# Kernel optimization log

Measured on AMD Instinct MI355X. Metric: run time of the kernel, lower is better.

Reference implementation:

```python
import jax, jax.numpy as jnp
import numpy as np

D = 256        # model_dim
E = 4          # num_experts
H = 8          # attention heads
L = 8          # layers
P = 4          # patch size
IMG = 128
B = 8
NUM_CLASSES = 10
T = (IMG // P) ** 2  # 1024 tokens


def _ln(x, g, b):
    mu = jnp.mean(x, -1, keepdims=True)
    var = jnp.mean((x - mu) ** 2, -1, keepdims=True)
    return (x - mu) * jax.lax.rsqrt(var + 1e-5) * g + b


def setup_inputs() -> dict:
    key = jax.random.key(0)
    ks = jax.random.split(key, 24)
    n = lambda k, s, sc=0.02: jax.random.normal(k, s, jnp.float32) * sc
    return {
        "x": jax.random.normal(ks[0], (B, 3, IMG, IMG), jnp.float32),
        "patch_w": n(ks[1], (D, 3, P, P), 0.1),
        "patch_b": n(ks[2], (D,), 0.01),
        "pos_emb": n(ks[3], (1, T, D), 0.02),
        "router_w": n(ks[4], (E, D), 0.05),
        "router_b": n(ks[5], (E,), 0.01),
        "ln1_g": jnp.ones((L, D), jnp.float32),
        "ln1_b": jnp.zeros((L, D), jnp.float32),
        "q_w": n(ks[6], (L, D, D), 0.05),
        "q_b": n(ks[7], (L, D), 0.01),
        "k_w": n(ks[8], (L, D, D), 0.05),
        "k_b": n(ks[9], (L, D), 0.01),
        "v_w": n(ks[10], (L, D, D), 0.05),
        "v_b": n(ks[11], (L, D), 0.01),
        "o_w": n(ks[12], (L, D, D), 0.05),
        "o_b": n(ks[13], (L, D), 0.01),
        "ln2_g": jnp.ones((L, D), jnp.float32),
        "ln2_b": jnp.zeros((L, D), jnp.float32),
        "l1_w": n(ks[14], (L, 4 * D, D), 0.05),
        "l1_b": n(ks[15], (L, 4 * D), 0.01),
        "l2_w": n(ks[16], (L, D, 4 * D), 0.05),
        "l2_b": n(ks[17], (L, D), 0.01),
        "head_w": n(ks[18], (NUM_CLASSES, D), 0.05),
        "head_b": n(ks[19], (NUM_CLASSES,), 0.01),
        "alpha": jnp.full((1,), 0.5, jnp.float32),
    }


def reference(x, patch_w, patch_b, pos_emb, router_w, router_b, ln1_g, ln1_b,
              q_w, q_b, k_w, k_b, v_w, v_b, o_w, o_b, ln2_g, ln2_b,
              l1_w, l1_b, l2_w, l2_b, head_w, head_b, alpha):
    b = x.shape[0]
    # patch embed: Conv2d(3, D, P, stride=P)
    h = jax.lax.conv_general_dilated(x, patch_w, (P, P), 'VALID',
                                     dimension_numbers=('NCHW', 'OIHW', 'NCHW'))
    h = h + patch_b[None, :, None, None]
    tok = h.reshape(b, D, -1).transpose(0, 2, 1) + pos_emb   # [B,T,D]
    t = tok.shape[1]
    n_per = t // E  # uniform capacity: floor(T * 1/E)
    raw_prob = jax.nn.softmax(tok @ router_w.T + router_b, axis=-1)  # [B,T,E]
    # greedy routing: expert e takes top n_per of remaining tokens, rows zeroed after
    prob = raw_prob
    bidx = jnp.arange(b)[:, None]
    blocks, pblocks = [], []
    for e in range(E):
        _, idx = jax.lax.top_k(prob[:, :, e], n_per)            # [B,n_per]
        blocks.append(jnp.take_along_axis(tok, idx[:, :, None], axis=1))
        pblocks.append(jnp.take_along_axis(raw_prob, idx[:, :, None], axis=1))
        sel = jnp.zeros((b, t), prob.dtype).at[bidx, idx].set(1.0)
        prob = prob * (1.0 - sel)[:, :, None]
    xs = jnp.concatenate(blocks, axis=1)    # [B,T,D] expert-sorted
    rp = jnp.concatenate(pblocks, axis=1)   # [B,T,E]

    widths = [D // 2 ** e for e in range(E)]  # [256,128,64,32]
    scale = D ** -0.5                         # note: model_dim, not head_dim
    dh = D // H
    for l in range(L):
        # ---- nested-expert MHSA ----
        xn = _ln(xs, ln1_g[l], ln1_b[l])
        qs, ks_, vs = [], [], []
        for e in range(E):
            m = widths[e]
            blk = xn[:, e * n_per:(e + 1) * n_per, :m]
            qs.append(blk @ q_w[l][:, :m].T + q_b[l])
            ks_.append(blk @ k_w[l][:, :m].T + k_b[l])
            vs.append(blk @ v_w[l][:, :m].T + v_b[l])
        q = jnp.concatenate(qs, 1).reshape(b, t, H, dh).transpose(0, 2, 1, 3)
        k = jnp.concatenate(ks_, 1).reshape(b, t, H, dh).transpose(0, 2, 1, 3)
        v = jnp.concatenate(vs, 1).reshape(b, t, H, dh).transpose(0, 2, 1, 3)
        attn = jax.nn.softmax(jnp.einsum('bhqd,bhkd->bhqk', q, k) * scale, axis=-1)
        ao = jnp.einsum('bhqk,bhkd->bhqd', attn, v).transpose(0, 2, 1, 3).reshape(b, t, D)
        outs = []
        for e in range(E):
            m = widths[e]
            sl = slice(e * n_per, (e + 1) * n_per)
            o = ao[:, sl, :m] @ o_w[l][:m, :m].T + o_b[l][:m]
            o = jnp.pad(o, ((0, 0), (0, 0), (0, D - m)))
            outs.append(o + xs[:, sl, :])
        xs = jnp.concatenate(outs, 1)
        # ---- nested-expert MLP ----
        xn = _ln(xs, ln2_g[l], ln2_b[l])
        outs = []
        for e in range(E):
            m = widths[e]
            sl = slice(e * n_per, (e + 1) * n_per)
            blk = xn[:, sl, :m]
            inner = jax.nn.gelu(blk @ l1_w[l][:, :m].T + l1_b[l], approximate=False)
            outer = inner @ l2_w[l][:m, :].T + l2_b[l][:m]
            outer = jnp.pad(outer, ((0, 0), (0, 0), (0, D - m)))
            sf = (alpha[0] * rp[:, sl, e] + 1.0)[:, :, None]
            outs.append(xs[:, sl, :] + sf * outer)
        xs = jnp.concatenate(outs, 1)
    # classification head: mean pool + linear
    return jnp.mean(xs, axis=1) @ head_w.T + head_b
```

## Files before the change

### kernel.cpp

```cpp
#include <hip/hip_runtime.h>
#include <math.h>

#define D 256
#define E 4
#define H 8
#define LYR 8
#define IMG 128
#define BB 8
#define NC 10
#define T 1024
#define NPER 256
#define DH 32
#define D4 1024

using bf16x8 = __attribute__((ext_vector_type(8))) __bf16;
using bf16x4 = __attribute__((ext_vector_type(4))) __bf16;
using f32x4  = __attribute__((ext_vector_type(4))) float;

#define MFMA16(a, b, c) __builtin_amdgcn_mfma_f32_16x16x32_bf16((a), (b), (c), 0, 0, 0)

__global__ void cast6(const float* __restrict__ s0, const float* __restrict__ s1,
                      const float* __restrict__ s2, const float* __restrict__ s3,
                      const float* __restrict__ s4, const float* __restrict__ s5,
                      __bf16* __restrict__ d0, __bf16* __restrict__ d1,
                      __bf16* __restrict__ d2, __bf16* __restrict__ d3,
                      __bf16* __restrict__ d4, __bf16* __restrict__ d5) {
    const long A4 = (long)LYR * D * D / 4;
    const long W4 = (long)LYR * D4 * D / 4;
    long i = (long)blockIdx.x * 256 + threadIdx.x;
    const float* s; __bf16* d; long off;
    if (i < 4 * A4) {
        int w = (int)(i / A4); off = i - (long)w * A4;
        s = w == 0 ? s0 : w == 1 ? s1 : w == 2 ? s2 : s3;
        d = w == 0 ? d0 : w == 1 ? d1 : w == 2 ? d2 : d3;
    } else {
        long j = i - 4 * A4;
        int w = (int)(j / W4); off = j - (long)w * W4;
        s = w ? s5 : s4; d = w ? d5 : d4;
    }
    float4 v = ((const float4*)s)[off];
    bf16x4 o;
    o[0] = (__bf16)v.x; o[1] = (__bf16)v.y; o[2] = (__bf16)v.z; o[3] = (__bf16)v.w;
    ((bf16x4*)d)[off] = o;
}

__global__ void patch_embed(const float* __restrict__ x, const float* __restrict__ pw,
                            const float* __restrict__ pb, const float* __restrict__ pos,
                            float* __restrict__ tok) {
    int t = blockIdx.x, b = blockIdx.y, d = threadIdx.x;
    __shared__ float sx[48];
    int ph = t >> 5, pwc = t & 31;
    if (d < 48) {
        int c = d >> 4, ij = d & 15, i = ij >> 2, j = ij & 3;
        sx[d] = x[(((long)b * 3 + c) * IMG + (ph * 4 + i)) * IMG + (pwc * 4 + j)];
    }
    __syncthreads();
    float acc = pb[d];
    #pragma unroll
    for (int kk = 0; kk < 48; ++kk) acc += sx[kk] * pw[d * 48 + kk];
    tok[((long)b * T + t) * D + d] = acc + pos[(long)t * D + d];
}

__global__ void router(const float* __restrict__ tok, const float* __restrict__ rw,
                       const float* __restrict__ rb, float* __restrict__ rawp) {
    int row = blockIdx.x;
    int lane = threadIdx.x;
    const float* tr = tok + (long)row * D;
    float a0 = 0.f, a1 = 0.f, a2 = 0.f, a3 = 0.f;
    for (int c = lane; c < D; c += 64) {
        float xv = tr[c];
        a0 += xv * rw[0 * D + c];
        a1 += xv * rw[1 * D + c];
        a2 += xv * rw[2 * D + c];
        a3 += xv * rw[3 * D + c];
    }
    for (int off = 32; off; off >>= 1) {
        a0 += __shfl_down(a0, off);
        a1 += __shfl_down(a1, off);
        a2 += __shfl_down(a2, off);
        a3 += __shfl_down(a3, off);
    }
    if (lane == 0) {
        float l0 = a0 + rb[0], l1 = a1 + rb[1], l2 = a2 + rb[2], l3 = a3 + rb[3];
        float mx = fmaxf(fmaxf(l0, l1), fmaxf(l2, l3));
        float e0 = __expf(l0 - mx), e1 = __expf(l1 - mx), e2 = __expf(l2 - mx), e3 = __expf(l3 - mx);
        float inv = 1.0f / (e0 + e1 + e2 + e3);
        rawp[(long)row * 4 + 0] = e0 * inv;
        rawp[(long)row * 4 + 1] = e1 * inv;
        rawp[(long)row * 4 + 2] = e2 * inv;
        rawp[(long)row * 4 + 3] = e3 * inv;
    }
}

__global__ __launch_bounds__(1024) void route_topk(const float* __restrict__ rawp,
                                                   int* __restrict__ perm,
                                                   float* __restrict__ rpsel) {
    int b = blockIdx.x, tid = threadIdx.x;
    int lane = tid & 63, wv = tid >> 6;
    __shared__ unsigned hist[256];
    __shared__ unsigned long long ball[16];
    __shared__ int sb_bin, sb_rem;
    bool assigned = false;
    for (int e = 0; e < E; ++e) {
        float v = rawp[((long)b * T + tid) * E + e];
        unsigned key = assigned ? 0u : __float_as_uint(v);
        unsigned prefix = 0;
        int rem = NPER;
        #pragma unroll
        for (int pass = 3; pass >= 0; --pass) {
            int shift = pass * 8;
            if (tid < 256) hist[tid] = 0;
            __syncthreads();
            bool active = (pass == 3) || ((key >> (shift + 8)) == prefix);
            if (active) atomicAdd(&hist[(key >> shift) & 255], 1u);
            __syncthreads();
            if (tid < 64) {
                unsigned c[4], psum = 0;
                #pragma unroll
                for (int u = 0; u < 4; ++u) { c[u] = hist[tid * 4 + u]; psum += c[u]; }
                unsigned suf = psum;
                #pragma unroll
                for (int off = 1; off < 64; off <<= 1) {
                    unsigned o = __shfl_down(suf, off);
                    if (tid + off < 64) suf += o;
                }
                unsigned El = suf - psum;
                if (El < (unsigned)rem && (unsigned)rem <= suf) {
                    unsigned cab = El;
                    #pragma unroll
                    for (int u = 3; u >= 0; --u) {
                        if ((unsigned)rem > cab && (unsigned)rem <= cab + c[u]) {
                            sb_bin = tid * 4 + u;
                            sb_rem = (int)((unsigned)rem - cab);
                        }
                        cab += c[u];
                    }
                }
            }
            __syncthreads();
            prefix = (prefix << 8) | (unsigned)sb_bin;
            rem = sb_rem;
        }
        unsigned t = prefix;
        bool is_tie = (!assigned) && (key == t);
        unsigned long long mbt = __ballot(is_tie);
        if (lane == 0) ball[wv] = mbt;
        __syncthreads();
        int tierank = 0;
        for (int w2 = 0; w2 < wv; ++w2) tierank += __popcll(ball[w2]);
        tierank += __popcll(mbt & ((1ULL << lane) - 1));
        bool sel = (!assigned) && ((key > t) || (is_tie && tierank < rem));
        __syncthreads();
        unsigned long long mbs = __ballot(sel);
        if (lane == 0) ball[wv] = mbs;
        __syncthreads();
        int rank = 0;
        for (int w2 = 0; w2 < wv; ++w2) rank += __popcll(ball[w2]);
        rank += __popcll(mbs & ((1ULL << lane) - 1));
        if (sel) {
            perm[(long)b * T + e * NPER + rank] = tid;
            rpsel[(long)b * T + e * NPER + rank] = v;
            assigned = true;
        }
        __syncthreads();
    }
}

__global__ void gather_tokens(const float* __restrict__ tok, const int* __restrict__ perm,
                              float* __restrict__ xs) {
    int slot = blockIdx.x, b = blockIdx.y, d = threadIdx.x;
    int src = perm[(long)b * T + slot];
    xs[((long)b * T + slot) * D + d] = tok[((long)b * T + src) * D + d];
}

__device__ __forceinline__ void ln_rows32(const float* __restrict__ src,
                                          const float* __restrict__ g,
                                          const float* __restrict__ bta,
                                          __bf16 (*slds)[264], int tid) {
    int sub = tid & 15, rowh = tid >> 4;
    int col0 = sub * 16;
    float gv[16], bv[16];
    #pragma unroll
    for (int u = 0; u < 4; ++u) {
        float4 gg = *(const float4*)&g[col0 + 4 * u];
        float4 bb = *(const float4*)&bta[col0 + 4 * u];
        gv[4*u] = gg.x; gv[4*u+1] = gg.y; gv[4*u+2] = gg.z; gv[4*u+3] = gg.w;
        bv[4*u] = bb.x; bv[4*u+1] = bb.y; bv[4*u+2] = bb.z; bv[4*u+3] = bb.w;
    }
    #pragma unroll
    for (int half = 0; half < 2; ++half) {
        int r = rowh + half * 16;
        const float* rp = src + (long)r * D + col0;
        float v[16];
        #pragma unroll
        for (int u = 0; u < 4; ++u) {
            float4 vv = *(const float4*)&rp[4 * u];
            v[4*u] = vv.x; v[4*u+1] = vv.y; v[4*u+2] = vv.z; v[4*u+3] = vv.w;
        }
        float s = 0.f;
        #pragma unroll
        for (int u = 0; u < 16; ++u) s += v[u];
        #pragma unroll
        for (int mk = 1; mk < 16; mk <<= 1) s += __shfl_xor(s, mk);
        float mu = s * (1.0f / D);
        float s2 = 0.f;
        #pragma unroll
        for (int u = 0; u < 16; ++u) { v[u] -= mu; s2 += v[u] * v[u]; }
        #pragma unroll
        for (int mk = 1; mk < 16; mk <<= 1) s2 += __shfl_xor(s2, mk);
        float rstd = rsqrtf(s2 * (1.0f / D) + 1e-5f);
        bf16x8 o0, o1;
        #pragma unroll
        for (int u = 0; u < 8; ++u) o0[u] = (__bf16)(v[u] * rstd * gv[u] + bv[u]);
        #pragma unroll
        for (int u = 0; u < 8; ++u) o1[u] = (__bf16)(v[8+u] * rstd * gv[8+u] + bv[8+u]);
        *(bf16x8*)&slds[r][col0]     = o0;
        *(bf16x8*)&slds[r][col0 + 8] = o1;
    }
}

__device__ __forceinline__ void gemm_tile(
    const __bf16* __restrict__ A, int lda,
    const __bf16* __restrict__ W, int ldb,
    int K, int lane, f32x4 acc[2][4])
{
    int lr = lane & 15, lk = (lane >> 4) * 8;
    const __bf16* a0 = A + (long)lr * lda + lk;
    const __bf16* a1 = a0 + 16 * lda;
    const __bf16* b0 = W + (long)lr * ldb + lk;
    const __bf16* b1 = b0 + 16 * ldb;
    const __bf16* b2 = b0 + 32 * ldb;
    const __bf16* b3 = b0 + 48 * ldb;
    #pragma unroll 2
    for (int k = 0; k < K; k += 32) {
        bf16x8 av0 = *(const bf16x8*)(a0 + k);
        bf16x8 av1 = *(const bf16x8*)(a1 + k);
        bf16x8 bv0 = *(const bf16x8*)(b0 + k);
        bf16x8 bv1 = *(const bf16x8*)(b1 + k);
        bf16x8 bv2 = *(const bf16x8*)(b2 + k);
        bf16x8 bv3 = *(const bf16x8*)(b3 + k);
        acc[0][0] = MFMA16(av0, bv0, acc[0][0]);
        acc[0][1] = MFMA16(av0, bv1, acc[0][1]);
        acc[0][2] = MFMA16(av0, bv2, acc[0][2]);
        acc[0][3] = MFMA16(av0, bv3, acc[0][3]);
        acc[1][0] = MFMA16(av1, bv0, acc[1][0]);
        acc[1][1] = MFMA16(av1, bv1, acc[1][1]);
        acc[1][2] = MFMA16(av1, bv2, acc[1][2]);
        acc[1][3] = MFMA16(av1, bv3, acc[1][3]);
    }
}

__global__ __launch_bounds__(256) void qkv_ln_gemm(
    const float* __restrict__ xs,
    const __bf16* __restrict__ qwb, const __bf16* __restrict__ kwb, const __bf16* __restrict__ vwb,
    const float* __restrict__ qb, const float* __restrict__ kb, const float* __restrict__ vb,
    const float* __restrict__ g, const float* __restrict__ bta,
    __bf16* __restrict__ Qb, __bf16* __restrict__ Kb, __bf16* __restrict__ Vt)
{
    int tid = threadIdx.x, lane = tid & 63, wid = tid >> 6;
    int tile = blockIdx.x, which = blockIdx.y, b = blockIdx.z;
    int row0 = tile * 32;
    int m = D >> (row0 >> 8);
    __shared__ __bf16 slds[32][264];
    ln_rows32(xs + ((long)b * T + row0) * D, g, bta, slds, tid);
    __syncthreads();
    const __bf16* W = which == 0 ? qwb : which == 1 ? kwb : vwb;
    const float* bias = which == 0 ? qb : which == 1 ? kb : vb;
    int ncol0 = wid * 64;
    const f32x4 vz = {0.f, 0.f, 0.f, 0.f};
    f32x4 acc[2][4];
    #pragma unroll
    for (int i = 0; i < 2; ++i) { acc[i][0]=vz; acc[i][1]=vz; acc[i][2]=vz; acc[i][3]=vz; }
    gemm_tile(&slds[0][0], 264, W + (long)ncol0 * D, D, m, lane, acc);
    int lr = lane & 15, rg = (lane >> 4) * 4;
    #pragma unroll
    for (int i = 0; i < 2; ++i) {
        int row = row0 + i * 16 + rg;
        #pragma unroll
        for (int j = 0; j < 4; ++j) {
            int n = ncol0 + j * 16 + lr;
            float bvs = bias[n];
            if (which == 2) {
                bf16x4 pk;
                #pragma unroll
                for (int r = 0; r < 4; ++r) pk[r] = (__bf16)(acc[i][j][r] + bvs);
                *(bf16x4*)&Vt[((long)b * D + n) * T + row] = pk;
            } else if (which == 0) {
                #pragma unroll
                for (int r = 0; r < 4; ++r)
                    Qb[((long)b * T + row + r) * D + n] = (__bf16)((acc[i][j][r] + bvs) * 0.0625f);
            } else {
                #pragma unroll
                for (int r = 0; r < 4; ++r)
                    Kb[((long)b * T + row + r) * D + n] = (__bf16)(acc[i][j][r] + bvs);
            }
        }
    }
}

__global__ __launch_bounds__(256) void attn_mfma(
    const __bf16* __restrict__ Qb, const __bf16* __restrict__ Kb,
    const __bf16* __restrict__ Vt, __bf16* __restrict__ aob)
{
    int bid = blockIdx.x;
    int bh = (bid & 7) * 8 + ((bid >> 3) & 7);
    int qt = bid >> 6;
    int b = bh >> 3, h = bh & 7;
    int lane = threadIdx.x & 63, wave = threadIdx.x >> 6;
    int lr = lane & 15, g = lane >> 4;
    int q0 = qt * 128 + wave * 32;
    __shared__ __bf16 plds[4][32][72];
    const f32x4 vz = {0.f, 0.f, 0.f, 0.f};
    bf16x8 qf[2];
    qf[0] = *(const bf16x8*)&Qb[((long)b * T + q0 + lr) * D + h * DH + g * 8];
    qf[1] = *(const bf16x8*)&Qb[((long)b * T + q0 + 16 + lr) * D + h * DH + g * 8];
    f32x4 acc[2][2] = {{vz, vz}, {vz, vz}};
    float ls[2] = {0.f, 0.f};
    const __bf16* kbase = Kb + (long)b * T * D + h * DH + g * 8;
    const __bf16* vbase = Vt + ((long)b * D + h * DH) * T;
    for (int kc = 0; kc < T; kc += 64) {
        bf16x8 kf[4];
        #pragma unroll
        for (int j = 0; j < 4; ++j)
            kf[j] = *(const bf16x8*)(kbase + (long)(kc + 16 * j + lr) * D);
        bf16x8 vf[2][2];
        #pragma unroll
        for (int w = 0; w < 2; ++w)
            #pragma unroll
            for (int df = 0; df < 2; ++df)
                vf[w][df] = *(const bf16x8*)(vbase + (long)(df * 16 + lr) * T + kc + 32 * w + 8 * g);
        #pragma unroll
        for (int qi = 0; qi < 2; ++qi) {
            #pragma unroll
            for (int j = 0; j < 4; ++j) {
                f32x4 s = MFMA16(kf[j], qf[qi], vz);
                float p0 = __expf(s[0]), p1 = __expf(s[1]);
                float p2 = __expf(s[2]), p3 = __expf(s[3]);
                ls[qi] += (p0 + p1) + (p2 + p3);
                bf16x4 pk;
                pk[0] = (__bf16)p0; pk[1] = (__bf16)p1;
                pk[2] = (__bf16)p2; pk[3] = (__bf16)p3;
                *(bf16x4*)&plds[wave][qi * 16 + lr][16 * j + 4 * g] = pk;
            }
        }
        #pragma unroll
        for (int qi = 0; qi < 2; ++qi) {
            #pragma unroll
            for (int w = 0; w < 2; ++w) {
                bf16x8 pa = *(const bf16x8*)&plds[wave][qi * 16 + lr][32 * w + 8 * g];
                acc[qi][0] = MFMA16(pa, vf[w][0], acc[qi][0]);
                acc[qi][1] = MFMA16(pa, vf[w][1], acc[qi][1]);
            }
        }
    }
    #pragma unroll
    for (int qi = 0; qi < 2; ++qi) {
        ls[qi] += __shfl_xor(ls[qi], 16);
        ls[qi] += __shfl_xor(ls[qi], 32);
        float inv = 1.0f / ls[qi];
        #pragma unroll
        for (int r = 0; r < 4; ++r) {
            float invr = __shfl(inv, 4 * g + r);
            long obase = ((long)b * T + q0 + qi * 16 + 4 * g + r) * D + h * DH;
            aob[obase + lr]      = (__bf16)(acc[qi][0][r] * invr);
            aob[obase + 16 + lr] = (__bf16)(acc[qi][1][r] * invr);
        }
    }
}

#define GEMM_PROLOGUE \
    int lane = threadIdx.x & 63, wid = threadIdx.x >> 6; \
    int wm = wid >> 1, wn = wid & 1; \
    int b = blockIdx.z >> 2, e = blockIdx.z & 3; \
    int m = D >> e; \
    const f32x4 vz = {0.f, 0.f, 0.f, 0.f}; \
    f32x4 acc[2][4]; \
    _Pragma("unroll") \
    for (int i = 0; i < 2; ++i) { acc[i][0]=vz; acc[i][1]=vz; acc[i][2]=vz; acc[i][3]=vz; }

__global__ __launch_bounds__(256) void oproj_gemm(
    const __bf16* __restrict__ aob, const __bf16* __restrict__ owb,
    const float* __restrict__ ob, float* __restrict__ xs)
{
    GEMM_PROLOGUE
    if ((int)blockIdx.y * 128 >= m) return;
    int ncol0 = blockIdx.y * 128 + wn * 64;
    int row0 = e * NPER + blockIdx.x * 64 + wm * 32;
    gemm_tile(aob + ((long)b * T + row0) * D, D, owb + (long)ncol0 * D, D, m, lane, acc);
    int lr = lane & 15, rg = (lane >> 4) * 4;
    #pragma unroll
    for (int i = 0; i < 2; ++i) {
        int row = row0 + i * 16 + rg;
        #pragma unroll
        for (int j = 0; j < 4; ++j) {
            int n = ncol0 + j * 16 + lr;
            if (n < m) {
                float bv = ob[n];
                #pragma unroll
                for (int r = 0; r < 4; ++r)
                    xs[((long)b * T + row + r) * D + n] += acc[i][j][r] + bv;
            }
        }
    }
}

__global__ __launch_bounds__(256) void mlp1_ln_gemm(
    const float* __restrict__ xs, const __bf16* __restrict__ w1b,
    const float* __restrict__ b1, const float* __restrict__ g, const float* __restrict__ bta,
    __bf16* __restrict__ innerb)
{
    int tid = threadIdx.x, lane = tid & 63, wid = tid >> 6;
    int tile = blockIdx.x, fq = blockIdx.y, b = blockIdx.z;
    int row0 = tile * 32;
    int m = D >> (row0 >> 8);
    __shared__ __bf16 slds[32][264];
    ln_rows32(xs + ((long)b * T + row0) * D, g, bta, slds, tid);
    __syncthreads();
    int ncol0 = fq * 256 + wid * 64;
    const f32x4 vz = {0.f, 0.f, 0.f, 0.f};
    f32x4 acc[2][4];
    #pragma unroll
    for (int i = 0; i < 2; ++i) { acc[i][0]=vz; acc[i][1]=vz; acc[i][2]=vz; acc[i][3]=vz; }
    gemm_tile(&slds[0][0], 264, w1b + (long)ncol0 * D, D, m, lane, acc);
    int lr = lane & 15, rg = (lane >> 4) * 4;
    #pragma unroll
    for (int i = 0; i < 2; ++i) {
        int row = row0 + i * 16 + rg;
        #pragma unroll
        for (int j = 0; j < 4; ++j) {
            int f = ncol0 + j * 16 + lr;
            float bv = b1[f];
            #pragma unroll
            for (int r = 0; r < 4; ++r) {
                float xv = acc[i][j][r] + bv;
                float gl = 0.5f * xv * (1.0f + erff(xv * 0.70710678118654752f));
                innerb[((long)b * T + row + r) * D4 + f] = (__bf16)gl;
            }
        }
    }
}

__global__ __launch_bounds__(256) void mlp2_gemm(
    const __bf16* __restrict__ innerb, const __bf16* __restrict__ w2b,
    const float* __restrict__ b2, const float* __restrict__ rpsel,
    const float* __restrict__ alpha, float* __restrict__ xs)
{
    GEMM_PROLOGUE
    if ((int)blockIdx.y * 128 >= m) return;
    int ncol0 = blockIdx.y * 128 + wn * 64;
    int row0 = e * NPER + blockIdx.x * 64 + wm * 32;
    gemm_tile(innerb + ((long)b * T + row0) * D4, D4, w2b + (long)ncol0 * D4, D4, D4, lane, acc);
    int lr = lane & 15, rg = (lane >> 4) * 4;
    float a0 = alpha[0];
    #pragma unroll
    for (int i = 0; i < 2; ++i) {
        int row = row0 + i * 16 + rg;
        float sf[4];
        #pragma unroll
        for (int r = 0; r < 4; ++r) sf[r] = a0 * rpsel[(long)b * T + row + r] + 1.0f;
        #pragma unroll
        for (int j = 0; j < 4; ++j) {
            int n = ncol0 + j * 16 + lr;
            if (n < m) {
                float bv = b2[n];
                #pragma unroll
                for (int r = 0; r < 4; ++r)
                    xs[((long)b * T + row + r) * D + n] += sf[r] * (acc[i][j][r] + bv);
            }
        }
    }
}

__global__ void head_partial(const float* __restrict__ xs, float* __restrict__ part) {
    int c = blockIdx.x, b = blockIdx.y, d = threadIdx.x;
    const float* p = xs + ((long)b * T + c * 128) * D + d;
    float s = 0.f;
    #pragma unroll 8
    for (int i = 0; i < 128; ++i) s += p[(long)i * D];
    part[((long)b * 8 + c) * D + d] = s;
}

__global__ void head_final(const float* __restrict__ part, const float* __restrict__ hw,
                           const float* __restrict__ hb, float* __restrict__ out) {
    int b = blockIdx.x, d = threadIdx.x;
    __shared__ float smean[D];
    float s = 0.f;
    #pragma unroll
    for (int c = 0; c < 8; ++c) s += part[((long)b * 8 + c) * D + d];
    smean[d] = s * (1.0f / T);
    __syncthreads();
    if (d < NC) {
        float acc = hb[d];
        for (int c = 0; c < D; ++c) acc += smean[c] * hw[d * D + c];
        out[b * NC + d] = acc;
    }
}

extern "C" void kernel_launch(void* const* d_in, const int* in_sizes, int n_in,
                              void* d_out, int out_size, void* d_ws, size_t ws_size,
                              hipStream_t stream) {
    const float* x      = (const float*)d_in[0];
    const float* patchw = (const float*)d_in[1];
    const float* patchb = (const float*)d_in[2];
    const float* pos    = (const float*)d_in[3];
    const float* rw     = (const float*)d_in[4];
    const float* rb     = (const float*)d_in[5];
    const float* ln1g   = (const float*)d_in[6];
    const float* ln1b   = (const float*)d_in[7];
    const float* qw     = (const float*)d_in[8];
    const float* qbi    = (const float*)d_in[9];
    const float* kw     = (const float*)d_in[10];
    const float* kbi    = (const float*)d_in[11];
    const float* vw     = (const float*)d_in[12];
    const float* vbi    = (const float*)d_in[13];
    const float* ow     = (const float*)d_in[14];
    const float* obi    = (const float*)d_in[15];
    const float* ln2g   = (const float*)d_in[16];
    const float* ln2b   = (const float*)d_in[17];
    const float* l1w    = (const float*)d_in[18];
    const float* l1b    = (const float*)d_in[19];
    const float* l2w    = (const float*)d_in[20];
    const float* l2b    = (const float*)d_in[21];
    const float* hw     = (const float*)d_in[22];
    const float* hb     = (const float*)d_in[23];
    const float* alpha  = (const float*)d_in[24];

    char* p = (char*)d_ws;
    auto alloc = [&](size_t bytes) { void* r = (void*)p; p += (bytes + 255) & ~(size_t)255; return r; };
    const long NTD = (long)BB * T * D;

    float*  tok    = (float*)alloc(NTD * 4);
    float*  xs     = (float*)alloc(NTD * 4);
    float*  rawp   = (float*)alloc((long)BB * T * E * 4);
    float*  rpsel  = (float*)alloc((long)BB * T * 4);
    int*    perm   = (int*)alloc((long)BB * T * 4);
    float*  part   = (float*)alloc((long)BB * 8 * D * 4);
    __bf16* Qb     = (__bf16*)alloc(NTD * 2);
    __bf16* Kb     = (__bf16*)alloc(NTD * 2);
    __bf16* Vt     = (__bf16*)alloc(NTD * 2);
    __bf16* aob    = (__bf16*)alloc(NTD * 2);
    __bf16* innerb = (__bf16*)alloc((long)BB * T * D4 * 2);
    __bf16* qwb    = (__bf16*)alloc((long)LYR * D * D * 2);
    __bf16* kwb    = (__bf16*)alloc((long)LYR * D * D * 2);
    __bf16* vwb    = (__bf16*)alloc((long)LYR * D * D * 2);
    __bf16* owb    = (__bf16*)alloc((long)LYR * D * D * 2);
    __bf16* w1b    = (__bf16*)alloc((long)LYR * D4 * D * 2);
    __bf16* w2b    = (__bf16*)alloc((long)LYR * D * D4 * 2);

    cast6<<<6144, 256, 0, stream>>>(qw, kw, vw, ow, l1w, l2w, qwb, kwb, vwb, owb, w1b, w2b);

    patch_embed<<<dim3(T, BB), D, 0, stream>>>(x, patchw, patchb, pos, tok);
    router<<<BB * T, 64, 0, stream>>>(tok, rw, rb, rawp);
    route_topk<<<BB, 1024, 0, stream>>>(rawp, perm, rpsel);
    gather_tokens<<<dim3(T, BB), D, 0, stream>>>(tok, perm, xs);

    for (int l = 0; l < LYR; ++l) {
        qkv_ln_gemm<<<dim3(32, 3, BB), 256, 0, stream>>>(
            xs, qwb + (long)l * D * D, kwb + (long)l * D * D, vwb + (long)l * D * D,
            qbi + l * D, kbi + l * D, vbi + l * D,
            ln1g + l * D, ln1b + l * D, Qb, Kb, Vt);
        attn_mfma<<<dim3(512), 256, 0, stream>>>(Qb, Kb, Vt, aob);
        oproj_gemm<<<dim3(4, 2, BB * E), 256, 0, stream>>>(
            aob, owb + (long)l * D * D, obi + l * D, xs);
        mlp1_ln_gemm<<<dim3(32, 4, BB), 256, 0, stream>>>(
            xs, w1b + (long)l * D4 * D, l1b + (long)l * D4,
            ln2g + l * D, ln2b + l * D, innerb);
        mlp2_gemm<<<dim3(4, 2, BB * E), 256, 0, stream>>>(
            innerb, w2b + (long)l * D * D4, l2b + l * D, rpsel, alpha, xs);
    }

    head_partial<<<dim3(8, BB), 256, 0, stream>>>(xs, part);
    head_final<<<BB, D, 0, stream>>>(part, hw, hb, (float*)d_out);
}
```

Measured before the change: 1.036 ms.

## Fuse patch embed with router, template GEMM K loop, halve attention query tile

Merges the patch embedding and router softmax into one kernel so the token row is reused from shared memory instead of being reread by a second launch. The GEMM tile helper now takes its K extent as a template parameter, dispatched on the expert width, so the inner loop can be fully unrolled in chunks. The attention kernel handles 16 query rows per wave instead of 32 and launches twice as many blocks, trading K/V reuse for more parallelism and lower register use.

```diff
diff --git a/kernel.cpp b/kernel.cpp
--- a/kernel.cpp
+++ b/kernel.cpp
@@ -44,11 +44,14 @@
     ((bf16x4*)d)[off] = o;
 }
 
-__global__ void patch_embed(const float* __restrict__ x, const float* __restrict__ pw,
-                            const float* __restrict__ pb, const float* __restrict__ pos,
-                            float* __restrict__ tok) {
+__global__ void patch_router(const float* __restrict__ x, const float* __restrict__ pw,
+                             const float* __restrict__ pb, const float* __restrict__ pos,
+                             const float* __restrict__ rw, const float* __restrict__ rb,
+                             float* __restrict__ tok, float* __restrict__ rawp) {
     int t = blockIdx.x, b = blockIdx.y, d = threadIdx.x;
     __shared__ float sx[48];
+    __shared__ float srow[D];
+    __shared__ float slog[4];
     int ph = t >> 5, pwc = t & 31;
     if (d < 48) {
         int c = d >> 4, ij = d & 15, i = ij >> 2, j = ij & 3;
@@ -58,37 +61,26 @@
     float acc = pb[d];
     #pragma unroll
     for (int kk = 0; kk < 48; ++kk) acc += sx[kk] * pw[d * 48 + kk];
-    tok[((long)b * T + t) * D + d] = acc + pos[(long)t * D + d];
-}
-
-__global__ void router(const float* __restrict__ tok, const float* __restrict__ rw,
-                       const float* __restrict__ rb, float* __restrict__ rawp) {
-    int row = blockIdx.x;
-    int lane = threadIdx.x;
-    const float* tr = tok + (long)row * D;
-    float a0 = 0.f, a1 = 0.f, a2 = 0.f, a3 = 0.f;
-    for (int c = lane; c < D; c += 64) {
-        float xv = tr[c];
-        a0 += xv * rw[0 * D + c];
-        a1 += xv * rw[1 * D + c];
-        a2 += xv * rw[2 * D + c];
-        a3 += xv * rw[3 * D + c];
-    }
-    for (int off = 32; off; off >>= 1) {
-        a0 += __shfl_down(a0, off);
-        a1 += __shfl_down(a1, off);
-        a2 += __shfl_down(a2, off);
-        a3 += __shfl_down(a3, off);
-    }
-    if (lane == 0) {
-        float l0 = a0 + rb[0], l1 = a1 + rb[1], l2 = a2 + rb[2], l3 = a3 + rb[3];
+    float val = acc + pos[(long)t * D + d];
+    tok[((long)b * T + t) * D + d] = val;
+    srow[d] = val;
+    __syncthreads();
+    int wv = d >> 6, lane = d & 63;
+    float a = 0.f;
+    for (int c = lane; c < D; c += 64) a += srow[c] * rw[wv * D + c];
+    for (int off = 32; off; off >>= 1) a += __shfl_down(a, off);
+    if (lane == 0) slog[wv] = a + rb[wv];
+    __syncthreads();
+    if (d == 0) {
+        float l0 = slog[0], l1 = slog[1], l2 = slog[2], l3 = slog[3];
         float mx = fmaxf(fmaxf(l0, l1), fmaxf(l2, l3));
         float e0 = __expf(l0 - mx), e1 = __expf(l1 - mx), e2 = __expf(l2 - mx), e3 = __expf(l3 - mx);
         float inv = 1.0f / (e0 + e1 + e2 + e3);
-        rawp[(long)row * 4 + 0] = e0 * inv;
-        rawp[(long)row * 4 + 1] = e1 * inv;
-        rawp[(long)row * 4 + 2] = e2 * inv;
-        rawp[(long)row * 4 + 3] = e3 * inv;
+        long row = (long)b * T + t;
+        rawp[row * 4 + 0] = e0 * inv;
+        rawp[row * 4 + 1] = e1 * inv;
+        rawp[row * 4 + 2] = e2 * inv;
+        rawp[row * 4 + 3] = e3 * inv;
     }
 }
 
@@ -219,36 +211,48 @@
     }
 }
 
+template<int RG, int K>
 __device__ __forceinline__ void gemm_tile(
     const __bf16* __restrict__ A, int lda,
     const __bf16* __restrict__ W, int ldb,
-    int K, int lane, f32x4 acc[2][4])
+    int lane, f32x4 (&acc)[RG][4])
 {
     int lr = lane & 15, lk = (lane >> 4) * 8;
     const __bf16* a0 = A + (long)lr * lda + lk;
-    const __bf16* a1 = a0 + 16 * lda;
     const __bf16* b0 = W + (long)lr * ldb + lk;
     const __bf16* b1 = b0 + 16 * ldb;
     const __bf16* b2 = b0 + 32 * ldb;
     const __bf16* b3 = b0 + 48 * ldb;
-    #pragma unroll 2
-    for (int k = 0; k < K; k += 32) {
-        bf16x8 av0 = *(const bf16x8*)(a0 + k);
-        bf16x8 av1 = *(const bf16x8*)(a1 + k);
-        bf16x8 bv0 = *(const bf16x8*)(b0 + k);
-        bf16x8 bv1 = *(const bf16x8*)(b1 + k);
-        bf16x8 bv2 = *(const bf16x8*)(b2 + k);
-        bf16x8 bv3 = *(const bf16x8*)(b3 + k);
-        acc[0][0] = MFMA16(av0, bv0, acc[0][0]);
-        acc[0][1] = MFMA16(av0, bv1, acc[0][1]);
-        acc[0][2] = MFMA16(av0, bv2, acc[0][2]);
-        acc[0][3] = MFMA16(av0, bv3, acc[0][3]);
-        acc[1][0] = MFMA16(av1, bv0, acc[1][0]);
-        acc[1][1] = MFMA16(av1, bv1, acc[1][1]);
-        acc[1][2] = MFMA16(av1, bv2, acc[1][2]);
-        acc[1][3] = MFMA16(av1, bv3, acc[1][3]);
-    }
-}
+    constexpr int CH = (K <= 256) ? K : 128;
+    for (int kb = 0; kb < K; kb += CH) {
+        #pragma unroll
+        for (int ku = 0; ku < CH; ku += 32) {
+            int k = kb + ku;
+            bf16x8 av[RG];
+            #pragma unroll
+            for (int i = 0; i < RG; ++i) av[i] = *(const bf16x8*)(a0 + i * 16 * lda + k);
+            bf16x8 bv0 = *(const bf16x8*)(b0 + k);
+            bf16x8 bv1 = *(const bf16x8*)(b1 + k);
+            bf16x8 bv2 = *(const bf16x8*)(b2 + k);
+            bf16x8 bv3 = *(const bf16x8*)(b3 + k);
+            #pragma unroll
+            for (int i = 0; i < RG; ++i) {
+                acc[i][0] = MFMA16(av[i], bv0, acc[i][0]);
+                acc[i][1] = MFMA16(av[i], bv1, acc[i][1]);
+                acc[i][2] = MFMA16(av[i], bv2, acc[i][2]);
+                acc[i][3] = MFMA16(av[i], bv3, acc[i][3]);
+            }
+        }
+    }
+}
+
+#define GEMM_K_DISPATCH(RG, Aexpr, lda, Wexpr, ldb, accv)                        \
+    switch (m) {                                                                 \
+      case 256: gemm_tile<RG, 256>(Aexpr, lda, Wexpr, ldb, lane, accv); break;   \
+      case 128: gemm_tile<RG, 128>(Aexpr, lda, Wexpr, ldb, lane, accv); break;   \
+      case 64:  gemm_tile<RG, 64>(Aexpr, lda, Wexpr, ldb, lane, accv); break;    \
+      default:  gemm_tile<RG, 32>(Aexpr, lda, Wexpr, ldb, lane, accv); break;    \
+    }
 
 __global__ __launch_bounds__(256) void qkv_ln_gemm(
     const float* __restrict__ xs,
@@ -271,7 +275,7 @@
     f32x4 acc[2][4];
     #pragma unroll
     for (int i = 0; i < 2; ++i) { acc[i][0]=vz; acc[i][1]=vz; acc[i][2]=vz; acc[i][3]=vz; }
-    gemm_tile(&slds[0][0], 264, W + (long)ncol0 * D, D, m, lane, acc);
+    GEMM_K_DISPATCH(2, &slds[0][0], 264, W + (long)ncol0 * D, D, acc)
     int lr = lane & 15, rg = (lane >> 4) * 4;
     #pragma unroll
     for (int i = 0; i < 2; ++i) {
@@ -303,19 +307,16 @@
     const __bf16* __restrict__ Vt, __bf16* __restrict__ aob)
 {
     int bid = blockIdx.x;
-    int bh = (bid & 7) * 8 + ((bid >> 3) & 7);
+    int b = bid & 7, h = (bid >> 3) & 7;
     int qt = bid >> 6;
-    int b = bh >> 3, h = bh & 7;
     int lane = threadIdx.x & 63, wave = threadIdx.x >> 6;
     int lr = lane & 15, g = lane >> 4;
-    int q0 = qt * 128 + wave * 32;
-    __shared__ __bf16 plds[4][32][72];
+    int q0 = qt * 64 + wave * 16;
+    __shared__ __bf16 plds[4][16][72];
     const f32x4 vz = {0.f, 0.f, 0.f, 0.f};
-    bf16x8 qf[2];
-    qf[0] = *(const bf16x8*)&Qb[((long)b * T + q0 + lr) * D + h * DH + g * 8];
-    qf[1] = *(const bf16x8*)&Qb[((long)b * T + q0 + 16 + lr) * D + h * DH + g * 8];
-    f32x4 acc[2][2] = {{vz, vz}, {vz, vz}};
-    float ls[2] = {0.f, 0.f};
+    bf16x8 qf = *(const bf16x8*)&Qb[((long)b * T + q0 + lr) * D + h * DH + g * 8];
+    f32x4 acc0 = vz, acc1 = vz;
+    float ls = 0.f;
     const __bf16* kbase = Kb + (long)b * T * D + h * DH + g * 8;
     const __bf16* vbase = Vt + ((long)b * D + h * DH) * T;
     for (int kc = 0; kc < T; kc += 64) {
@@ -323,48 +324,39 @@
         #pragma unroll
         for (int j = 0; j < 4; ++j)
             kf[j] = *(const bf16x8*)(kbase + (long)(kc + 16 * j + lr) * D);
-        bf16x8 vf[2][2];
-        #pragma unroll
-        for (int w = 0; w < 2; ++w)
-            #pragma unroll
-            for (int df = 0; df < 2; ++df)
-                vf[w][df] = *(const bf16x8*)(vbase + (long)(df * 16 + lr) * T + kc + 32 * w + 8 * g);
-        #pragma unroll
-        for (int qi = 0; qi < 2; ++qi) {
-            #pragma unroll
-            for (int j = 0; j < 4; ++j) {
-                f32x4 s = MFMA16(kf[j], qf[qi], vz);
-                float p0 = __expf(s[0]), p1 = __expf(s[1]);
-                float p2 = __expf(s[2]), p3 = __expf(s[3]);
-                ls[qi] += (p0 + p1) + (p2 + p3);
-                bf16x4 pk;
-                pk[0] = (__bf16)p0; pk[1] = (__bf16)p1;
-                pk[2] = (__bf16)p2; pk[3] = (__bf16)p3;
-                *(bf16x4*)&plds[wave][qi * 16 + lr][16 * j + 4 * g] = pk;
-            }
-        }
-        #pragma unroll
-        for (int qi = 0; qi < 2; ++qi) {
-            #pragma unroll
-            for (int w = 0; w < 2; ++w) {
-                bf16x8 pa = *(const bf16x8*)&plds[wave][qi * 16 + lr][32 * w + 8 * g];
-                acc[qi][0] = MFMA16(pa, vf[w][0], acc[qi][0]);
-                acc[qi][1] = MFMA16(pa, vf[w][1], acc[qi][1]);
-            }
-        }
-    }
-    #pragma unroll
-    for (int qi = 0; qi < 2; ++qi) {
-        ls[qi] += __shfl_xor(ls[qi], 16);
-        ls[qi] += __shfl_xor(ls[qi], 32);
-        float inv = 1.0f / ls[qi];
-        #pragma unroll
-        for (int r = 0; r < 4; ++r) {
-            float invr = __shfl(inv, 4 * g + r);
-            long obase = ((long)b * T + q0 + qi * 16 + 4 * g + r) * D + h * DH;
-            aob[obase + lr]      = (__bf16)(acc[qi][0][r] * invr);
-            aob[obase + 16 + lr] = (__bf16)(acc[qi][1][r] * invr);
-        }
+        bf16x8 vf0[2], vf1[2];
+        #pragma unroll
+        for (int w = 0; w < 2; ++w) {
+            vf0[w] = *(const bf16x8*)(vbase + (long)lr * T        + kc + 32 * w + 8 * g);
+            vf1[w] = *(const bf16x8*)(vbase + (long)(16 + lr) * T + kc + 32 * w + 8 * g);
+        }
+        #pragma unroll
+        for (int j = 0; j < 4; ++j) {
+            f32x4 s = MFMA16(kf[j], qf, vz);
+            float p0 = __expf(s[0]), p1 = __expf(s[1]);
+            float p2 = __expf(s[2]), p3 = __expf(s[3]);
+            ls += (p0 + p1) + (p2 + p3);
+            bf16x4 pk;
+            pk[0] = (__bf16)p0; pk[1] = (__bf16)p1;
+            pk[2] = (__bf16)p2; pk[3] = (__bf16)p3;
+            *(bf16x4*)&plds[wave][lr][16 * j + 4 * g] = pk;
+        }
+        #pragma unroll
+        for (int w = 0; w < 2; ++w) {
+            bf16x8 pa = *(const bf16x8*)&plds[wave][lr][32 * w + 8 * g];
+            acc0 = MFMA16(pa, vf0[w], acc0);
+            acc1 = MFMA16(pa, vf1[w], acc1);
+        }
+    }
+    ls += __shfl_xor(ls, 16);
+    ls += __shfl_xor(ls, 32);
+    float inv = 1.0f / ls;
+    #pragma unroll
+    for (int r = 0; r < 4; ++r) {
+        float invr = __shfl(inv, 4 * g + r);
+        long obase = ((long)b * T + q0 + 4 * g + r) * D + h * DH;
+        aob[obase + lr]      = (__bf16)(acc0[r] * invr);
+        aob[obase + 16 + lr] = (__bf16)(acc1[r] * invr);
     }
 }
 
@@ -386,7 +378,7 @@
     if ((int)blockIdx.y * 128 >= m) return;
     int ncol0 = blockIdx.y * 128 + wn * 64;
     int row0 = e * NPER + blockIdx.x * 64 + wm * 32;
-    gemm_tile(aob + ((long)b * T + row0) * D, D, owb + (long)ncol0 * D, D, m, lane, acc);
+    GEMM_K_DISPATCH(2, aob + ((long)b * T + row0) * D, D, owb + (long)ncol0 * D, D, acc)
     int lr = lane & 15, rg = (lane >> 4) * 4;
     #pragma unroll
     for (int i = 0; i < 2; ++i) {
@@ -421,7 +413,7 @@
     f32x4 acc[2][4];
     #pragma unroll
     for (int i = 0; i < 2; ++i) { acc[i][0]=vz; acc[i][1]=vz; acc[i][2]=vz; acc[i][3]=vz; }
-    gemm_tile(&slds[0][0], 264, w1b + (long)ncol0 * D, D, m, lane, acc);
+    GEMM_K_DISPATCH(2, &slds[0][0], 264, w1b + (long)ncol0 * D, D, acc)
     int lr = lane & 15, rg = (lane >> 4) * 4;
     #pragma unroll
     for (int i = 0; i < 2; ++i) {
@@ -449,7 +441,8 @@
     if ((int)blockIdx.y * 128 >= m) return;
     int ncol0 = blockIdx.y * 128 + wn * 64;
     int row0 = e * NPER + blockIdx.x * 64 + wm * 32;
-    gemm_tile(innerb + ((long)b * T + row0) * D4, D4, w2b + (long)ncol0 * D4, D4, D4, lane, acc);
+    gemm_tile<2, 1024>(innerb + ((long)b * T + row0) * D4, D4,
+                       w2b + (long)ncol0 * D4, D4, lane, acc);
     int lr = lane & 15, rg = (lane >> 4) * 4;
     float a0 = alpha[0];
     #pragma unroll
@@ -549,17 +542,16 @@
 
     cast6<<<6144, 256, 0, stream>>>(qw, kw, vw, ow, l1w, l2w, qwb, kwb, vwb, owb, w1b, w2b);
 
-    patch_embed<<<dim3(T, BB), D, 0, stream>>>(x, patchw, patchb, pos, tok);
-    router<<<BB * T, 64, 0, stream>>>(tok, rw, rb, rawp);
+    patch_router<<<dim3(T, BB), 256, 0, stream>>>(x, patchw, patchb, pos, rw, rb, tok, rawp);
     route_topk<<<BB, 1024, 0, stream>>>(rawp, perm, rpsel);
-    gather_tokens<<<dim3(T, BB), D, 0, stream>>>(tok, perm, xs);
+    gather_tokens<<<dim3(T, BB), 256, 0, stream>>>(tok, perm, xs);
 
     for (int l = 0; l < LYR; ++l) {
         qkv_ln_gemm<<<dim3(32, 3, BB), 256, 0, stream>>>(
             xs, qwb + (long)l * D * D, kwb + (long)l * D * D, vwb + (long)l * D * D,
             qbi + l * D, kbi + l * D, vbi + l * D,
             ln1g + l * D, ln1b + l * D, Qb, Kb, Vt);
-        attn_mfma<<<dim3(512), 256, 0, stream>>>(Qb, Kb, Vt, aob);
+        attn_mfma<<<dim3(1024), 256, 0, stream>>>(Qb, Kb, Vt, aob);
         oproj_gemm<<<dim3(4, 2, BB * E), 256, 0, stream>>>(
             aob, owb + (long)l * D * D, obi + l * D, xs);
         mlp1_ln_gemm<<<dim3(32, 4, BB), 256, 0, stream>>>(
```

After: 1.257 ms. 1.21x slower.
